# Optimization experiments

Hardware: AMD Instinct MI355X
Metric: run time of the kernel (lower is better)

The kernel has to match this reference:

```python
import jax, jax.numpy as jnp
import numpy as np

N_NODES = 100000


def gcn_conv(x, W, b, src, dst, num_nodes):
    """PyG GCNConv: self-loops + symmetric norm + linear + scatter-add."""
    loop = jnp.arange(num_nodes, dtype=src.dtype)
    s = jnp.concatenate([src, loop])  # [E+N]
    d = jnp.concatenate([dst, loop])  # [E+N]
    # degree on destination column (edge_weight = 1)
    deg = jax.ops.segment_sum(jnp.ones_like(d, dtype=x.dtype), d,
                              num_segments=num_nodes)
    dinv = jnp.where(deg > 0, jax.lax.rsqrt(deg), 0.0)
    norm = dinv[s] * dinv[d]  # [E+N]
    h = x @ W  # [N, out] project before aggregation
    msg = h[s] * norm[:, None]  # gather + normalize
    out = jax.ops.segment_sum(msg, d, num_segments=num_nodes)  # scatter-add
    return out + b


def setup_inputs() -> dict:
    key = jax.random.key(0)
    k_x, k_e, k_w1, k_b1, k_w2, k_b2 = jax.random.split(key, 6)
    in_channels, hidden, out_dim = 128, 64, 2
    n_edges = 3200000
    x = jax.random.normal(k_x, (N_NODES, in_channels), dtype=jnp.float32)
    edge_index = jax.random.randint(k_e, (2, n_edges), 0, N_NODES, dtype=jnp.int64)
    # Glorot-style init for linear weights, zero bias (PyG default)
    W1 = jax.random.normal(k_w1, (in_channels, hidden), dtype=jnp.float32) * (1.0 / np.sqrt(in_channels))
    b1 = jnp.zeros((hidden,), dtype=jnp.float32)
    W2 = jax.random.normal(k_w2, (hidden, out_dim), dtype=jnp.float32) * (1.0 / np.sqrt(hidden))
    b2 = jnp.zeros((out_dim,), dtype=jnp.float32)
    return {"x": x, "edge_index": edge_index, "W1": W1, "b1": b1, "W2": W2, "b2": b2}


def reference(x, edge_index, W1, b1, W2, b2):
    src, dst = edge_index[0], edge_index[1]
    h = gcn_conv(x, W1, b1, src, dst, N_NODES)
    h = jax.nn.relu(h)
    # dropout(p=0.3) is identity in eval mode
    return gcn_conv(h, W2, b2, src, dst, N_NODES)
```

## Files before the change

kernel.cpp:

```cpp
#include <hip/hip_runtime.h>
#include <hip/hip_fp16.h>

#define IN_CH 128
#define HID 64
#define CHUNK1 16384
#define GBITS 8
#define SCAN_CHUNK 8192

__global__ __launch_bounds__(512) void k_p1count(const int* __restrict__ dst,
                                                 int* __restrict__ C,
                                                 int E, int G, int NB1) {
    __shared__ int lcnt[512];
    int t = threadIdx.x;
    for (int i = t; i < G; i += 512) lcnt[i] = 0;
    __syncthreads();
    int lo = blockIdx.x * CHUNK1;
    int hi = min(E, lo + CHUNK1);
    for (int e = lo + t; e < hi; e += 512) {
        int d = __builtin_nontemporal_load(dst + e);
        atomicAdd(&lcnt[d >> GBITS], 1);
    }
    __syncthreads();
    for (int g = t; g < G; g += 512) C[(size_t)g * NB1 + blockIdx.x] = lcnt[g];
}

__global__ __launch_bounds__(256) void k_scan_blocksum(const int* __restrict__ a,
                                                       int* __restrict__ bsum, int M) {
    int t = threadIdx.x;
    int base = blockIdx.x * SCAN_CHUNK + t * 32;
    int s = 0;
#pragma unroll
    for (int q = 0; q < 8; ++q) {
        int b = base + q * 4;
        if (b + 3 < M) {
            int4 v = *(const int4*)(a + b);
            s += v.x + v.y + v.z + v.w;
        } else {
            for (int i = 0; i < 4; ++i) if (b + i < M) s += a[b + i];
        }
    }
#pragma unroll
    for (int off = 32; off; off >>= 1) s += __shfl_down(s, off);
    __shared__ int ws[4];
    if ((t & 63) == 0) ws[t >> 6] = s;
    __syncthreads();
    if (t == 0) bsum[blockIdx.x] = ws[0] + ws[1] + ws[2] + ws[3];
}

__global__ __launch_bounds__(128) void k_scan_bsums(int* __restrict__ bsum, int nb) {
    __shared__ int sh[128];
    int t = threadIdx.x;
    int v = (t < nb) ? bsum[t] : 0;
    sh[t] = v;
    __syncthreads();
    for (int off = 1; off < 128; off <<= 1) {
        int u = (t >= off) ? sh[t - off] : 0;
        __syncthreads();
        sh[t] += u;
        __syncthreads();
    }
    if (t < nb) bsum[t] = (t == 0) ? 0 : sh[t - 1];
}

__global__ __launch_bounds__(256) void k_scan_apply(int* __restrict__ a,
                                                    const int* __restrict__ boff,
                                                    int M, int E) {
    int t = threadIdx.x;
    int base = blockIdx.x * SCAN_CHUNK + t * 32;
    int v[32];
    int tsum = 0;
#pragma unroll
    for (int q = 0; q < 8; ++q) {
        int b = base + q * 4;
        if (b + 3 < M) {
            int4 w = *(const int4*)(a + b);
            v[q * 4 + 0] = w.x; v[q * 4 + 1] = w.y; v[q * 4 + 2] = w.z; v[q * 4 + 3] = w.w;
        } else {
            for (int i = 0; i < 4; ++i) v[q * 4 + i] = (b + i < M) ? a[b + i] : 0;
        }
        tsum += v[q * 4] + v[q * 4 + 1] + v[q * 4 + 2] + v[q * 4 + 3];
    }
    __shared__ int sh[256];
    sh[t] = tsum;
    __syncthreads();
    for (int off = 1; off < 256; off <<= 1) {
        int u = (t >= off) ? sh[t - off] : 0;
        __syncthreads();
        sh[t] += u;
        __syncthreads();
    }
    int run = ((t == 0) ? 0 : sh[t - 1]) + boff[blockIdx.x];
#pragma unroll
    for (int q = 0; q < 8; ++q) {
        int b = base + q * 4;
        int o0 = run;            run += v[q * 4 + 0];
        int o1 = run;            run += v[q * 4 + 1];
        int o2 = run;            run += v[q * 4 + 2];
        int o3 = run;            run += v[q * 4 + 3];
        if (b + 3 < M) { *(int4*)(a + b) = make_int4(o0, o1, o2, o3); }
        else {
            if (b     < M) a[b]     = o0;
            if (b + 1 < M) a[b + 1] = o1;
            if (b + 2 < M) a[b + 2] = o2;
            if (b + 3 < M) a[b + 3] = o3;
        }
    }
    if (blockIdx.x == 0 && t == 0) a[M] = E;
}

__global__ __launch_bounds__(512) void k_p1scat(const int* __restrict__ src,
                                                const int* __restrict__ dst,
                                                const int* __restrict__ S,
                                                unsigned int* __restrict__ part,
                                                int E, int G, int NB1) {
    __shared__ int lcur[512];
    int t = threadIdx.x;
    for (int g = t; g < G; g += 512) lcur[g] = S[(size_t)g * NB1 + blockIdx.x];
    __syncthreads();
    int lo = blockIdx.x * CHUNK1;
    int hi = min(E, lo + CHUNK1);
    for (int e = lo + t; e < hi; e += 512) {
        int d = __builtin_nontemporal_load(dst + e);
        int s = __builtin_nontemporal_load(src + e);
        int pos = atomicAdd(&lcur[d >> GBITS], 1);
        part[pos] = ((unsigned)s << GBITS) | (unsigned)(d & ((1 << GBITS) - 1));
    }
}

__global__ __launch_bounds__(512) void k_p2(const unsigned int* __restrict__ part,
                                            const int* __restrict__ S,
                                            int* __restrict__ rowptr,
                                            float* __restrict__ dinv,
                                            int* __restrict__ esorted,
                                            int E, int N, int G, int NB1) {
    __shared__ int lcnt[256], lpre[256], lexc[256];
    int t = threadIdx.x;
    int g = blockIdx.x;
    int base = S[(size_t)g * NB1];
    int end  = (g == G - 1) ? E : S[(size_t)(g + 1) * NB1];
    if (t < 256) lcnt[t] = 0;
    __syncthreads();
    unsigned int  ed[18];
    unsigned char rk[18];
#pragma unroll
    for (int q = 0; q < 18; ++q) {
        int i = base + t + q * 512;
        if (i < end) {
            unsigned p = part[i];
            ed[q] = p;
            rk[q] = (unsigned char)atomicAdd(&lcnt[p & 255], 1);
        }
    }
    __syncthreads();
    int v = 0;
    if (t < 256) { v = lcnt[t]; lpre[t] = v; }
    __syncthreads();
    for (int off = 1; off < 256; off <<= 1) {
        int u = (t >= off && t < 256) ? lpre[t - off] : 0;
        __syncthreads();
        if (t < 256) lpre[t] += u;
        __syncthreads();
    }
    if (t < 256) {
        int excl = lpre[t] - v;
        lexc[t] = excl;
        int node = (g << GBITS) + t;
        if (node < N) {
            rowptr[node] = base + excl;
            dinv[node] = rsqrtf(1.0f + (float)v);
        }
    }
    if (g == 0 && t == 0) rowptr[N] = E;
    __syncthreads();
#pragma unroll
    for (int q = 0; q < 18; ++q) {
        int i = base + t + q * 512;
        if (i < end) {
            unsigned p = ed[q];
            esorted[base + lexc[p & 255] + (int)rk[q]] = (int)(p >> GBITS);
        }
    }
}

__global__ __launch_bounds__(256) void k_gemm1(const float* __restrict__ x,
                                               const float* __restrict__ W1,
                                               const float* __restrict__ dinv,
                                               __half* __restrict__ hp1h, int N) {
    __shared__ float sW[IN_CH * HID];
    __shared__ float sx[16 * IN_CH];
    const int tid = threadIdx.x;
    const int node0 = blockIdx.x * 16;

    {
        const float4* g = (const float4*)W1;
        float4* s = (float4*)sW;
        for (int i = tid; i < IN_CH * HID / 4; i += 256) s[i] = g[i];
    }
    {
        const float4* g = (const float4*)(x + (size_t)node0 * IN_CH);
        float4* s = (float4*)sx;
        for (int i = tid; i < 16 * IN_CH / 4; i += 256) s[i] = g[i];
    }
    __syncthreads();

    const int k  = tid & 63;
    const int n0 = tid >> 6;
    float a0 = 0.f, a1 = 0.f, a2 = 0.f, a3 = 0.f;
#pragma unroll 8
    for (int j = 0; j < IN_CH; ++j) {
        float w = sW[j * HID + k];
        a0 = fmaf(sx[(n0     ) * IN_CH + j], w, a0);
        a1 = fmaf(sx[(n0 +  4) * IN_CH + j], w, a1);
        a2 = fmaf(sx[(n0 +  8) * IN_CH + j], w, a2);
        a3 = fmaf(sx[(n0 + 12) * IN_CH + j], w, a3);
    }
    hp1h[(size_t)(node0 + n0     ) * HID + k] = __float2half(a0 * dinv[node0 + n0]);
    hp1h[(size_t)(node0 + n0 +  4) * HID + k] = __float2half(a1 * dinv[node0 + n0 + 4]);
    hp1h[(size_t)(node0 + n0 +  8) * HID + k] = __float2half(a2 * dinv[node0 + n0 + 8]);
    hp1h[(size_t)(node0 + n0 + 12) * HID + k] = __float2half(a3 * dinv[node0 + n0 + 12]);
}

__global__ __launch_bounds__(256) void k_agg1(const int* __restrict__ rowptr,
                                              const int* __restrict__ esorted,
                                              const __half2* __restrict__ hp1h,
                                              const float* __restrict__ dinv,
                                              const float* __restrict__ b1,
                                              const float* __restrict__ W2,
                                              float* __restrict__ hp2, int N) {
    int wid = (blockIdx.x * blockDim.x + threadIdx.x) >> 6;
    if (wid >= N) return;
    const int lane = threadIdx.x & 63;
    const int k32  = lane & 31;
    const int half = lane >> 5;
    int beg = rowptr[wid], end = rowptr[wid + 1];

    float ax = 0.f, ay = 0.f;
    int e = beg;
    for (; e + 31 < end; e += 32) {
        const int* ep = esorted + e + 16 * half;
        int s0 = ep[0],  s1 = ep[1],  s2 = ep[2],  s3 = ep[3];
        int s4 = ep[4],  s5 = ep[5],  s6 = ep[6],  s7 = ep[7];
        int s8 = ep[8],  s9 = ep[9],  sa = ep[10], sb = ep[11];
        int sc = ep[12], sd = ep[13], se = ep[14], sf = ep[15];
        __half2 g0 = hp1h[(unsigned)(s0 * 32 + k32)];
        __half2 g1 = hp1h[(unsigned)(s1 * 32 + k32)];
        __half2 g2 = hp1h[(unsigned)(s2 * 32 + k32)];
        __half2 g3 = hp1h[(unsigned)(s3 * 32 + k32)];
        __half2 g4 = hp1h[(unsigned)(s4 * 32 + k32)];
        __half2 g5 = hp1h[(unsigned)(s5 * 32 + k32)];
        __half2 g6 = hp1h[(unsigned)(s6 * 32 + k32)];
        __half2 g7 = hp1h[(unsigned)(s7 * 32 + k32)];
        __half2 g8 = hp1h[(unsigned)(s8 * 32 + k32)];
        __half2 g9 = hp1h[(unsigned)(s9 * 32 + k32)];
        __half2 ga = hp1h[(unsigned)(sa * 32 + k32)];
        __half2 gb = hp1h[(unsigned)(sb * 32 + k32)];
        __half2 gc = hp1h[(unsigned)(sc * 32 + k32)];
        __half2 gd = hp1h[(unsigned)(sd * 32 + k32)];
        __half2 ge = hp1h[(unsigned)(se * 32 + k32)];
        __half2 gf = hp1h[(unsigned)(sf * 32 + k32)];
        __half2 h0 = __hadd2(g0, g4), h1 = __hadd2(g1, g5);
        __half2 h2 = __hadd2(g2, g6), h3 = __hadd2(g3, g7);
        float2 f0 = __half22float2(__hadd2(h0, h1));
        float2 f1 = __half22float2(__hadd2(h2, h3));
        __half2 h4 = __hadd2(g8, gc), h5 = __hadd2(g9, gd);
        __half2 h6 = __hadd2(ga, ge), h7 = __hadd2(gb, gf);
        float2 f2 = __half22float2(__hadd2(h4, h5));
        float2 f3 = __half22float2(__hadd2(h6, h7));
        ax += (f0.x + f1.x) + (f2.x + f3.x);
        ay += (f0.y + f1.y) + (f2.y + f3.y);
    }
    for (; e + 15 < end; e += 16) {
        const int* ep = esorted + e + 8 * half;
        int s0 = ep[0], s1 = ep[1], s2 = ep[2], s3 = ep[3];
        int s4 = ep[4], s5 = ep[5], s6 = ep[6], s7 = ep[7];
        __half2 h0 = hp1h[(unsigned)(s0 * 32 + k32)];
        __half2 h1 = hp1h[(unsigned)(s1 * 32 + k32)];
        __half2 h2 = hp1h[(unsigned)(s2 * 32 + k32)];
        __half2 h3 = hp1h[(unsigned)(s3 * 32 + k32)];
        h0 = __hadd2(h0, hp1h[(unsigned)(s4 * 32 + k32)]);
        h1 = __hadd2(h1, hp1h[(unsigned)(s5 * 32 + k32)]);
        h2 = __hadd2(h2, hp1h[(unsigned)(s6 * 32 + k32)]);
        h3 = __hadd2(h3, hp1h[(unsigned)(s7 * 32 + k32)]);
        float2 f0 = __half22float2(__hadd2(h0, h1));
        float2 f1 = __half22float2(__hadd2(h2, h3));
        ax += f0.x + f1.x;
        ay += f0.y + f1.y;
    }
    for (; e + 1 < end; e += 2) {
        int s = esorted[e + half];
        float2 f = __half22float2(hp1h[(unsigned)(s * 32 + k32)]);
        ax += f.x;
        ay += f.y;
    }
    if (e < end) {
        int s = esorted[e];
        float2 f = __half22float2(hp1h[(unsigned)(s * 32 + k32)]);
        if (half == 0) { ax += f.x; ay += f.y; }
    }
    ax += __shfl_xor(ax, 32);
    ay += __shfl_xor(ay, 32);

    float2 fs = __half22float2(hp1h[(unsigned)(wid * 32 + k32)]);
    ax += fs.x;
    ay += fs.y;

    float dj = dinv[wid];
    float2 bb = *(const float2*)(b1 + 2 * k32);
    float h0 = fmaxf(fmaf(dj, ax, bb.x), 0.0f);
    float h1 = fmaxf(fmaf(dj, ay, bb.y), 0.0f);
    float4 w4 = *(const float4*)(W2 + 4 * k32);
    float p0 = h0 * w4.x + h1 * w4.z;
    float p1 = h0 * w4.y + h1 * w4.w;
#pragma unroll
    for (int off = 32; off; off >>= 1) {
        p0 += __shfl_xor(p0, off);
        p1 += __shfl_xor(p1, off);
    }
    if (lane == 0) {
        hp2[(size_t)wid * 2 + 0] = p0 * 0.5f * dj;
        hp2[(size_t)wid * 2 + 1] = p1 * 0.5f * dj;
    }
}

__global__ __launch_bounds__(256) void k_agg2(const int* __restrict__ rowptr,
                                              const int* __restrict__ esorted,
                                              const float* __restrict__ hp2,
                                              const float* __restrict__ dinv,
                                              const float* __restrict__ b2,
                                              float* __restrict__ out, int N) {
    int gid = blockIdx.x * blockDim.x + threadIdx.x;
    int j = gid >> 3;
    if (j >= N) return;
    int l = gid & 7;
    int beg = rowptr[j], end = rowptr[j + 1];
    float ax = 0.f, ay = 0.f;
    for (int e = beg + l; e < end; e += 8) {
        int s = esorted[e];
        float2 v = *(const float2*)(hp2 + (size_t)s * 2);
        ax += v.x;
        ay += v.y;
    }
#pragma unroll
    for (int off = 1; off < 8; off <<= 1) {
        ax += __shfl_xor(ax, off);
        ay += __shfl_xor(ay, off);
    }
    if (l == 0) {
        float2 self = *(const float2*)(hp2 + (size_t)j * 2);
        float dj = dinv[j];
        out[(size_t)j * 2 + 0] = fmaf(dj, ax + self.x, b2[0]);
        out[(size_t)j * 2 + 1] = fmaf(dj, ay + self.y, b2[1]);
    }
}

extern "C" void kernel_launch(void* const* d_in, const int* in_sizes, int n_in,
                              void* d_out, int out_size, void* d_ws, size_t ws_size,
                              hipStream_t stream) {
    const float* x  = (const float*)d_in[0];
    const int*   ei = (const int*)d_in[1];
    const float* W1 = (const float*)d_in[2];
    const float* b1 = (const float*)d_in[3];
    const float* W2 = (const float*)d_in[4];
    const float* b2 = (const float*)d_in[5];
    float* out = (float*)d_out;

    const int N = in_sizes[0] / IN_CH;
    const int E = in_sizes[1] / 2;
    const int* src = ei;
    const int* dst = ei + E;

    const int G   = (N + 255) >> GBITS;
    const int NB1 = (E + CHUNK1 - 1) / CHUNK1;
    const int M   = G * NB1;
    const int NBs = (M + SCAN_CHUNK - 1) / SCAN_CHUNK;

    char* ws = (char*)d_ws;
    size_t o = 0;
    auto carve = [&](size_t bytes) -> char* {
        char* p = ws + o;
        o = (o + bytes + 255) & ~(size_t)255;
        return p;
    };
    int*          S       = (int*)carve(((size_t)M + 1) * 4);
    unsigned int* part    = (unsigned int*)carve((size_t)E * 4);
    int*          rowptr  = (int*)carve(((size_t)N + 1) * 4);
    float*        dinv    = (float*)carve((size_t)N * 4);
    int*          bsum    = (int*)carve(128 * 4);
    int*          esorted = (int*)carve((size_t)E * 4);
    __half*       hp1h    = (__half*)carve((size_t)N * HID * 2);
    float*        hp2     = (float*)carve((size_t)N * 2 * 4);
    (void)ws_size;

    k_p1count<<<NB1, 512, 0, stream>>>(dst, S, E, G, NB1);
    k_scan_blocksum<<<NBs, 256, 0, stream>>>(S, bsum, M);
    k_scan_bsums<<<1, 128, 0, stream>>>(bsum, NBs);
    k_scan_apply<<<NBs, 256, 0, stream>>>(S, bsum, M, E);
    k_p1scat<<<NB1, 512, 0, stream>>>(src, dst, S, part, E, G, NB1);
    k_p2<<<G, 512, 0, stream>>>(part, S, rowptr, dinv, esorted, E, N, G, NB1);

    k_gemm1<<<(N + 15) / 16, 256, 0, stream>>>(x, W1, dinv, hp1h, N);
    k_agg1<<<(unsigned)(((size_t)N * 64 + 255) / 256), 256, 0, stream>>>(
        rowptr, esorted, (const __half2*)hp1h, dinv, b1, W2, hp2, N);
    k_agg2<<<(unsigned)(((size_t)N * 8 + 255) / 256), 256, 0, stream>>>(
        rowptr, esorted, hp2, dinv, b2, out, N);
}
```

Measured before the change: 231.3 us.

## Make gemm1 persistent, halve partition chunk size, drop 32-edge agg1 unroll

k_gemm1 becomes a grid-stride persistent kernel with 512 blocks, so each block loads W1 into shared memory once and reuses it across many 16-node tiles instead of reloading it per tile. The partition chunk size CHUNK1 is halved, which doubles the number of count/scatter blocks and the size of the count matrix to be scanned. The 32-edge unrolled gather loop in k_agg1 is removed, leaving the 16-edge loop as the widest path, which cuts register pressure but lowers memory-level parallelism per wave. The persistent loop only covers N/16 full tiles, so a partial tail tile would be skipped; N=100000 divides evenly by 16.

```diff
diff --git a/kernel.cpp b/kernel.cpp
--- a/kernel.cpp
+++ b/kernel.cpp
@@ -3,7 +3,7 @@
 
 #define IN_CH 128
 #define HID 64
-#define CHUNK1 16384
+#define CHUNK1 8192
 #define GBITS 8
 #define SCAN_CHUNK 8192
 
@@ -189,35 +189,37 @@
     __shared__ float sW[IN_CH * HID];
     __shared__ float sx[16 * IN_CH];
     const int tid = threadIdx.x;
-    const int node0 = blockIdx.x * 16;
-
     {
         const float4* g = (const float4*)W1;
         float4* s = (float4*)sW;
         for (int i = tid; i < IN_CH * HID / 4; i += 256) s[i] = g[i];
     }
-    {
-        const float4* g = (const float4*)(x + (size_t)node0 * IN_CH);
-        float4* s = (float4*)sx;
-        for (int i = tid; i < 16 * IN_CH / 4; i += 256) s[i] = g[i];
-    }
-    __syncthreads();
-
     const int k  = tid & 63;
     const int n0 = tid >> 6;
-    float a0 = 0.f, a1 = 0.f, a2 = 0.f, a3 = 0.f;
+    const int ntiles = N / 16;
+    for (int tile = blockIdx.x; tile < ntiles; tile += gridDim.x) {
+        const int node0 = tile * 16;
+        __syncthreads();
+        {
+            const float4* g = (const float4*)(x + (size_t)node0 * IN_CH);
+            float4* s = (float4*)sx;
+            for (int i = tid; i < 16 * IN_CH / 4; i += 256) s[i] = g[i];
+        }
+        __syncthreads();
+        float a0 = 0.f, a1 = 0.f, a2 = 0.f, a3 = 0.f;
 #pragma unroll 8
-    for (int j = 0; j < IN_CH; ++j) {
-        float w = sW[j * HID + k];
-        a0 = fmaf(sx[(n0     ) * IN_CH + j], w, a0);
-        a1 = fmaf(sx[(n0 +  4) * IN_CH + j], w, a1);
-        a2 = fmaf(sx[(n0 +  8) * IN_CH + j], w, a2);
-        a3 = fmaf(sx[(n0 + 12) * IN_CH + j], w, a3);
-    }
-    hp1h[(size_t)(node0 + n0     ) * HID + k] = __float2half(a0 * dinv[node0 + n0]);
-    hp1h[(size_t)(node0 + n0 +  4) * HID + k] = __float2half(a1 * dinv[node0 + n0 + 4]);
-    hp1h[(size_t)(node0 + n0 +  8) * HID + k] = __float2half(a2 * dinv[node0 + n0 + 8]);
-    hp1h[(size_t)(node0 + n0 + 12) * HID + k] = __float2half(a3 * dinv[node0 + n0 + 12]);
+        for (int j = 0; j < IN_CH; ++j) {
+            float w = sW[j * HID + k];
+            a0 = fmaf(sx[(n0     ) * IN_CH + j], w, a0);
+            a1 = fmaf(sx[(n0 +  4) * IN_CH + j], w, a1);
+            a2 = fmaf(sx[(n0 +  8) * IN_CH + j], w, a2);
+            a3 = fmaf(sx[(n0 + 12) * IN_CH + j], w, a3);
+        }
+        hp1h[(size_t)(node0 + n0     ) * HID + k] = __float2half(a0 * dinv[node0 + n0]);
+        hp1h[(size_t)(node0 + n0 +  4) * HID + k] = __float2half(a1 * dinv[node0 + n0 + 4]);
+        hp1h[(size_t)(node0 + n0 +  8) * HID + k] = __float2half(a2 * dinv[node0 + n0 + 8]);
+        hp1h[(size_t)(node0 + n0 + 12) * HID + k] = __float2half(a3 * dinv[node0 + n0 + 12]);
+    }
 }
 
 __global__ __launch_bounds__(256) void k_agg1(const int* __restrict__ rowptr,
@@ -236,39 +238,6 @@
 
     float ax = 0.f, ay = 0.f;
     int e = beg;
-    for (; e + 31 < end; e += 32) {
-        const int* ep = esorted + e + 16 * half;
-        int s0 = ep[0],  s1 = ep[1],  s2 = ep[2],  s3 = ep[3];
-        int s4 = ep[4],  s5 = ep[5],  s6 = ep[6],  s7 = ep[7];
-        int s8 = ep[8],  s9 = ep[9],  sa = ep[10], sb = ep[11];
-        int sc = ep[12], sd = ep[13], se = ep[14], sf = ep[15];
-        __half2 g0 = hp1h[(unsigned)(s0 * 32 + k32)];
-        __half2 g1 = hp1h[(unsigned)(s1 * 32 + k32)];
-        __half2 g2 = hp1h[(unsigned)(s2 * 32 + k32)];
-        __half2 g3 = hp1h[(unsigned)(s3 * 32 + k32)];
-        __half2 g4 = hp1h[(unsigned)(s4 * 32 + k32)];
-        __half2 g5 = hp1h[(unsigned)(s5 * 32 + k32)];
-        __half2 g6 = hp1h[(unsigned)(s6 * 32 + k32)];
-        __half2 g7 = hp1h[(unsigned)(s7 * 32 + k32)];
-        __half2 g8 = hp1h[(unsigned)(s8 * 32 + k32)];
-        __half2 g9 = hp1h[(unsigned)(s9 * 32 + k32)];
-        __half2 ga = hp1h[(unsigned)(sa * 32 + k32)];
-        __half2 gb = hp1h[(unsigned)(sb * 32 + k32)];
-        __half2 gc = hp1h[(unsigned)(sc * 32 + k32)];
-        __half2 gd = hp1h[(unsigned)(sd * 32 + k32)];
-        __half2 ge = hp1h[(unsigned)(se * 32 + k32)];
-        __half2 gf = hp1h[(unsigned)(sf * 32 + k32)];
-        __half2 h0 = __hadd2(g0, g4), h1 = __hadd2(g1, g5);
-        __half2 h2 = __hadd2(g2, g6), h3 = __hadd2(g3, g7);
-        float2 f0 = __half22float2(__hadd2(h0, h1));
-        float2 f1 = __half22float2(__hadd2(h2, h3));
-        __half2 h4 = __hadd2(g8, gc), h5 = __hadd2(g9, gd);
-        __half2 h6 = __hadd2(ga, ge), h7 = __hadd2(gb, gf);
-        float2 f2 = __half22float2(__hadd2(h4, h5));
-        float2 f3 = __half22float2(__hadd2(h6, h7));
-        ax += (f0.x + f1.x) + (f2.x + f3.x);
-        ay += (f0.y + f1.y) + (f2.y + f3.y);
-    }
     for (; e + 15 < end; e += 16) {
         const int* ep = esorted + e + 8 * half;
         int s0 = ep[0], s1 = ep[1], s2 = ep[2], s3 = ep[3];
@@ -398,7 +367,7 @@
     k_p1scat<<<NB1, 512, 0, stream>>>(src, dst, S, part, E, G, NB1);
     k_p2<<<G, 512, 0, stream>>>(part, S, rowptr, dinv, esorted, E, N, G, NB1);
 
-    k_gemm1<<<(N + 15) / 16, 256, 0, stream>>>(x, W1, dinv, hp1h, N);
+    k_gemm1<<<512, 256, 0, stream>>>(x, W1, dinv, hp1h, N);
     k_agg1<<<(unsigned)(((size_t)N * 64 + 255) / 256), 256, 0, stream>>>(
         rowptr, esorted, (const __half2*)hp1h, dinv, b1, W2, hp2, N);
     k_agg2<<<(unsigned)(((size_t)N * 8 + 255) / 256), 256, 0, stream>>>(
```

Result: slower. 244.7 us (+5.8%).
